# Kernel optimization log

Hardware: AMD Instinct MI355X
Metric: run time of the kernel (lower is better)

## Reference

```python
import jax, jax.numpy as jnp
import numpy as np

VAR0, VAR1 = 0.1, 0.2       # variances used by encode()
THRESH = 0.35               # overlap_thresh
NEGPOS = 7                  # negpos_ratio


def point_form(p):
    # (cx,cy,w,h) -> (xmin,ymin,xmax,ymax)
    return jnp.concatenate([p[:, :2] - p[:, 2:] / 2, p[:, :2] + p[:, 2:] / 2], axis=1)


def jaccard(a, b):
    # a:[G,4], b:[P,4] corner form -> IoU [G,P]
    lt = jnp.maximum(a[:, None, :2], b[None, :, :2])
    rb = jnp.minimum(a[:, None, 2:], b[None, :, 2:])
    wh = jnp.clip(rb - lt, 0.0, None)
    inter = wh[..., 0] * wh[..., 1]
    area_a = (a[:, 2] - a[:, 0]) * (a[:, 3] - a[:, 1])
    area_b = (b[:, 2] - b[:, 0]) * (b[:, 3] - b[:, 1])
    return inter / (area_a[:, None] + area_b[None, :] - inter)


def encode(matched, priors):
    g_cxcy = ((matched[:, :2] + matched[:, 2:]) / 2 - priors[:, :2]) / (VAR0 * priors[:, 2:])
    g_wh = jnp.log((matched[:, 2:] - matched[:, :2]) / priors[:, 2:]) / VAR1
    return jnp.concatenate([g_cxcy, g_wh], axis=1)


def encode_landm(matched, priors):
    m = matched.reshape(-1, 5, 2)                                  # [P,5,2]
    g = (m - priors[:, None, :2]) / (VAR0 * priors[:, None, 2:])
    return g.reshape(-1, 10)


def match_one(truths, labels, landms, priors, priors_pf):
    # truths:[G,4] labels:[G] landms:[G,10] priors:[P,4](cxcywh) priors_pf:[P,4](corner)
    G = truths.shape[0]
    P = priors.shape[0]
    ov = jaccard(truths, priors_pf)                                # [G,P]
    best_prior_ov = ov.max(axis=1)                                 # [G]
    best_prior_idx = ov.argmax(axis=1)                             # [G]
    valid_gt = best_prior_ov >= 0.2
    best_truth_ov = ov.max(axis=0)                                 # [P]
    best_truth_idx = ov.argmax(axis=0)                             # [P]
    # index_fill_(0, best_prior_idx[valid_gt], 2): 2 > any IoU, so max is equivalent
    forced_ov = jnp.zeros((P,), ov.dtype).at[best_prior_idx].max(jnp.where(valid_gt, 2.0, 0.0))
    best_truth_ov = jnp.maximum(best_truth_ov, forced_ov)
    forced_idx = jnp.full((P,), -1, jnp.int32).at[best_prior_idx].max(jnp.arange(G, dtype=jnp.int32))
    best_truth_idx = jnp.where(forced_idx >= 0, forced_idx, best_truth_idx.astype(jnp.int32))
    conf = labels[best_truth_idx].astype(jnp.int32)
    conf = jnp.where(best_truth_ov < THRESH, 0, conf)
    loc = encode(truths[best_truth_idx], priors)                   # [P,4]
    landm = encode_landm(landms[best_truth_idx], priors)           # [P,10]
    # if no valid gt, torch zeroes the targets for this sample
    any_valid = valid_gt.any()
    loc = jnp.where(any_valid, loc, 0.0)
    landm = jnp.where(any_valid, landm, 0.0)
    conf = jnp.where(any_valid, conf, 0)
    return loc, conf, landm


def smooth_l1(x):
    ax = jnp.abs(x)
    return jnp.where(ax < 1.0, 0.5 * ax * ax, ax - 0.5)


def setup_inputs() -> dict:
    key = jax.random.key(0)
    k1, k2, k3, k4, k5, k6, k7, k8, k9 = jax.random.split(key, 9)
    B, P, G, C = 64, 16800, 32, 2
    cls_data = jax.random.normal(k1, (B, P, C), jnp.float32)
    loc_data = jax.random.normal(k2, (B, P, 4), jnp.float32)
    landm_data = jax.random.normal(k3, (B, P, 10), jnp.float32)
    # priors in (cx,cy,w,h), w,h in [0.02,0.3]
    pc = jax.random.uniform(k4, (P, 2), jnp.float32)
    pwh = jax.random.uniform(k5, (P, 2), jnp.float32, 0.02, 0.3)
    priors = jnp.concatenate([pc, pwh], axis=1)
    # targets: [B,G,15] = 4 box (corner form, valid) + 10 landmarks + 1 label
    c = jax.random.uniform(k6, (B, G, 2), jnp.float32, 0.15, 0.85)
    s = jax.random.uniform(k7, (B, G, 2), jnp.float32, 0.02, 0.3)
    boxes = jnp.concatenate([c - s / 2, c + s / 2], axis=-1)
    lms = jax.random.uniform(k8, (B, G, 10), jnp.float32)
    labels = jnp.where(jax.random.uniform(k9, (B, G, 1)) < 0.3, -1.0, 1.0)
    targets = jnp.concatenate([boxes, lms, labels], axis=-1)
    return {"cls_data": cls_data, "loc_data": loc_data, "landm_data": landm_data,
            "priors": priors, "targets": targets}


def reference(cls_data, loc_data, landm_data, priors, targets):
    truths = targets[:, :, :4]
    landms = targets[:, :, 4:14]
    labels = targets[:, :, 14]
    priors_pf = point_form(priors)
    loc_t, conf_t, landm_t = jax.vmap(
        lambda t, l, lm: match_one(t, l, lm, priors, priors_pf))(truths, labels, landms)
    num, P = conf_t.shape

    # landmark loss (smooth L1 over conf_t > 0)
    pos1 = conf_t > 0
    N1 = jnp.maximum(pos1.sum().astype(jnp.float32), 1.0)
    loss_landm = jnp.sum(smooth_l1(landm_data - landm_t) * pos1[..., None].astype(landm_data.dtype))

    # localization loss (smooth L1 over conf_t != 0)
    pos = conf_t != 0
    conf_t = jnp.where(pos, 1, conf_t)                              # conf_t[pos] = 1
    loss_l = jnp.sum(smooth_l1(loc_data - loc_t) * pos[..., None].astype(loc_data.dtype))

    # hard negative mining on per-prior CE loss
    logz = jax.nn.logsumexp(cls_data, axis=-1)                      # [B,P]
    gold = jnp.take_along_axis(cls_data, conf_t[..., None], axis=-1)[..., 0]
    loss_c = jnp.where(pos, 0.0, logz - gold)
    loss_idx = jnp.argsort(-loss_c, axis=1)
    idx_rank = jnp.argsort(loss_idx, axis=1)
    num_pos = pos.sum(axis=1, keepdims=True)
    num_neg = jnp.clip(NEGPOS * num_pos, None, P - 1)
    neg = idx_rank < num_neg

    sel = (pos | neg).astype(cls_data.dtype)
    loss_conf = jnp.sum((logz - gold) * sel)

    N = jnp.maximum(num_pos.sum().astype(jnp.float32), 1.0)
    return loss_l / N, loss_conf / N, loss_landm / N1
```

## Files before the change

### kernel.cpp

```cpp
#include <hip/hip_runtime.h>
#include <hip/hip_bf16.h>
#include <math.h>


#define RCP(x) __builtin_amdgcn_rcpf(x)
typedef unsigned long long u64;

constexpr int GN = 32;
constexpr int PACKF = 576;

__device__ __forceinline__ float sl1(float x) {
    float a = fabsf(x);
    return a < 1.f ? 0.5f * a * a : a - 0.5f;
}

constexpr int GPB = 4;
constexpr int GNT = 1024;
__global__ __launch_bounds__(GNT)
void k_gt(const float4* __restrict__ priors, const float* __restrict__ targets,
          u64* __restrict__ keys, float* __restrict__ pack,
          int* __restrict__ done, int P, int G) {
    const int b = blockIdx.y, g0 = blockIdx.x * GPB, tid = threadIdx.x;
    const int lane = tid & 63, w = tid >> 6;
    if (blockIdx.x == 0 && blockIdx.y == 0 && tid == 0) *done = 0;
    __shared__ float4 s_box[GPB];
    __shared__ float  s_at[GPB];
    __shared__ u64 s_wk[GNT / 64][GPB];
    if (tid < GPB) {
        const float* t = targets + ((size_t)b * G + g0 + tid) * 15;
        float4 v = make_float4(t[0], t[1], t[2], t[3]);
        float at = (v.z - v.x) * (v.w - v.y);
        s_box[tid] = v;
        s_at[tid] = at;
        float* pk = pack + (size_t)b * PACKF;
        ((float4*)pk)[g0 + tid] = v;
        pk[128 + g0 + tid] = 0.35f * at;
        pk[160 + g0 + tid] = at;
        pk[192 + g0 + tid] = t[14];
    }
    {
        int q = tid - GPB;
        if (q >= 0 && q < GPB * 10) {
            int gg = g0 + q / 10, j = q % 10;
            pack[(size_t)b * PACKF + 224 + gg * 10 + j] =
                targets[((size_t)b * G + gg) * 15 + 4 + j];
        }
    }
    __syncthreads();
    float4 tb0 = s_box[0], tb1 = s_box[1], tb2 = s_box[2], tb3 = s_box[3];
    float at0 = s_at[0], at1 = s_at[1], at2 = s_at[2], at3 = s_at[3];

    float bv[GPB]; int bp[GPB];
    #pragma unroll
    for (int j = 0; j < GPB; ++j) { bv[j] = -1.f; bp[j] = 0; }

    for (int p = tid; p < P; p += GNT) {
        float4 pr = priors[p];
        float hx = pr.z * 0.5f, hy = pr.w * 0.5f;
        float px0 = pr.x - hx, py0 = pr.y - hy;
        float px1 = pr.x + hx, py1 = pr.y + hy;
        float ap = (px1 - px0) * (py1 - py0);
        #pragma unroll
        for (int j = 0; j < GPB; ++j) {
            float4 tb = j == 0 ? tb0 : (j == 1 ? tb1 : (j == 2 ? tb2 : tb3));
            float at = j == 0 ? at0 : (j == 1 ? at1 : (j == 2 ? at2 : at3));
            float lx = fmaxf(tb.x, px0), ly = fmaxf(tb.y, py0);
            float rx = fminf(tb.z, px1), ry = fminf(tb.w, py1);
            float iw = fmaxf(rx - lx, 0.f), ih = fmaxf(ry - ly, 0.f);
            float inter = iw * ih;
            float iou = inter * RCP(at + ap - inter);
            if (iou > bv[j]) { bv[j] = iou; bp[j] = p; }
        }
    }
    #pragma unroll
    for (int j = 0; j < GPB; ++j) {
        u64 key = ((u64)__float_as_uint(bv[j]) << 32) | ~(unsigned)bp[j];
        #pragma unroll
        for (int o = 32; o > 0; o >>= 1) {
            u64 t = __shfl_down(key, o, 64);
            if (t > key) key = t;
        }
        if (lane == 0) s_wk[w][j] = key;
    }
    __syncthreads();
    if (tid < GPB) {
        u64 m = 0ull;
        #pragma unroll
        for (int q = 0; q < GNT / 64; ++q) { u64 t = s_wk[q][tid]; if (t > m) m = t; }
        keys[b * G + g0 + tid] = m;
    }
}

__global__ __launch_bounds__(256)
void k_match(const float2* __restrict__ cls, const float4* __restrict__ loc,
             const float* __restrict__ lmd, const float4* __restrict__ priors,
             const float* __restrict__ pack, const u64* __restrict__ keys,
             float* __restrict__ bc, float* __restrict__ part, int P, int NB) {
    const int b = blockIdx.y, bx = blockIdx.x, tid = threadIdx.x;
    const int lane = tid & 63, w = tid >> 6;
    const float* __restrict__ pk = pack + (size_t)b * PACKF;
    const float4* __restrict__ gbox = (const float4*)pk;
    const float* __restrict__ gc35 = pk + 128;
    const float* __restrict__ garea = pk + 160;
    const float* __restrict__ glab = pk + 192;
    const float* __restrict__ glm  = pk + 224;

    __shared__ int s_fg[256];
    __shared__ int s_fv[256];
    __shared__ unsigned s_vm;
    __shared__ float s_red[4][8];

    s_fg[tid] = -1; s_fv[tid] = 0;
    __syncthreads();
    if (tid < GN) {
        u64 key = keys[b * GN + tid];
        unsigned bp = ~(unsigned)key;
        bool val = __uint_as_float((unsigned)(key >> 32)) >= 0.2f;
        u64 bal = __ballot(val);
        if (tid == 0) s_vm = (unsigned)bal;
        int local = (int)bp - bx * 256;
        if (local >= 0 && local < 256) {
            atomicMax(&s_fg[local], tid);
            if (val) atomicOr(&s_fv[local], 1);
        }
    }
    __syncthreads();
    const bool av = s_vm != 0u;

    int p = bx * 256 + tid;
    const bool act = p < P;
    float2 c = act ? cls[(size_t)b * P + p] : make_float2(0.f, 0.f);
    float4 pr = act ? priors[p] : make_float4(0.f, 0.f, 0.f, 0.f);
    float hx = pr.z * 0.5f, hy = pr.w * 0.5f;
    float px0 = pr.x - hx, py0 = pr.y - hy;
    float px1 = pr.x + hx, py1 = pr.y + hy;
    float ap = (px1 - px0) * (py1 - py0);
    float ap35 = 0.35f * ap;

    float qmax = -INFINITY;
    #pragma unroll
    for (int g = 0; g < GN; ++g) {
        float4 tb = gbox[g];
        float lx = fmaxf(tb.x, px0), ly = fmaxf(tb.y, py0);
        float rx = fminf(tb.z, px1), ry = fminf(tb.w, py1);
        float iw = fmaxf(rx - lx, 0.f), ih = fmaxf(ry - ly, 0.f);
        qmax = fmaxf(qmax, fmaf(1.35f, iw * ih, -gc35[g]));
    }
    bool thr = act && (qmax >= ap35);
    int fidx = s_fg[tid];
    bool fv = s_fv[tid] != 0;
    bool pos = act && av && (fv || thr);

    float lse = 0.f, d = 0.f;
    if (act) {
        d = c.y - c.x;
        float m0 = fmaxf(d, 0.f);
        lse = m0 + __logf(__expf(-m0) + __expf(d - m0));
        bc[(size_t)b * P + p] = pos ? 0.f : lse;
    }

    float a_ll = 0.f, a_lm = 0.f, a_lcp = 0.f;
    bool posl = false;
    if (pos) {
        a_lcp = lse - d;
        int bti2 = fidx;
        if (fidx < 0) {
            float btv = -1.f;
            #pragma unroll 1
            for (int g = 0; g < GN; ++g) {
                float4 tb = gbox[g];
                float lx = fmaxf(tb.x, px0), ly = fmaxf(tb.y, py0);
                float rx = fminf(tb.z, px1), ry = fminf(tb.w, py1);
                float iw = fmaxf(rx - lx, 0.f), ih = fmaxf(ry - ly, 0.f);
                float inter = iw * ih;
                float iou = inter * RCP(garea[g] + ap - inter);
                if (iou > btv) { btv = iou; bti2 = g; }
            }
        }
        float4 tb = gbox[bti2];
        float rw = RCP(pr.z), rh = RCP(pr.w);
        float e0 = ((tb.x + tb.z) * 0.5f - pr.x) * rw * 10.f;
        float e1 = ((tb.y + tb.w) * 0.5f - pr.y) * rh * 10.f;
        float e2 = __logf((tb.z - tb.x) * rw) * 5.f;
        float e3 = __logf((tb.w - tb.y) * rh) * 5.f;
        float4 ld = loc[(size_t)b * P + p];
        a_ll = sl1(ld.x - e0) + sl1(ld.y - e1) + sl1(ld.z - e2) + sl1(ld.w - e3);
        if (glab[bti2] > 0.f) {
            posl = true;
            const float* lp = lmd + ((size_t)b * P + p) * 10;
            #pragma unroll
            for (int q = 0; q < 5; ++q) {
                float gx = (glm[bti2 * 10 + 2 * q]     - pr.x) * rw * 10.f;
                float gy = (glm[bti2 * 10 + 2 * q + 1] - pr.y) * rh * 10.f;
                a_lm += sl1(lp[2 * q] - gx) + sl1(lp[2 * q + 1] - gy);
            }
        }
    }

    u64 bpos = __ballot(pos);
    int npw  = __popcll(bpos);
    int np1w = __popcll(__ballot(posl));
    if (bpos) {
        #pragma unroll
        for (int o = 32; o > 0; o >>= 1) {
            a_ll  += __shfl_down(a_ll,  o, 64);
            a_lm  += __shfl_down(a_lm,  o, 64);
            a_lcp += __shfl_down(a_lcp, o, 64);
        }
    }
    if (lane == 0) {
        s_red[w][0] = a_ll; s_red[w][1] = a_lm; s_red[w][2] = a_lcp;
        s_red[w][3] = (float)npw; s_red[w][4] = (float)np1w;
    }
    __syncthreads();
    if (tid == 0) {
        float* pp = part + ((size_t)b * NB + bx) * 8;
        #pragma unroll
        for (int j = 0; j < 5; ++j)
            pp[j] = s_red[0][j] + s_red[1][j] + s_red[2][j] + s_red[3][j];
    }
}

constexpr int KNT = 1024;
constexpr int KNI = 17;
__global__ __launch_bounds__(KNT)
void k_select(const float* __restrict__ bc, const float* __restrict__ part,
              float* __restrict__ part2, float* __restrict__ out,
              int* __restrict__ done, int P, int NB, int B) {
    const int b = blockIdx.x, tid = threadIdx.x;
    const int lane = tid & 63, w = tid >> 6;
    __shared__ float s_r[5];
    __shared__ u64   s_cw[16];
    __shared__ u64   s_ct;
    __shared__ float s_rf[16][2];
    __shared__ float s_ts2[2];
    __shared__ int   s_last;

    unsigned ul[KNI];
    #pragma unroll
    for (int i = 0; i < KNI; ++i) {
        int idx = i * KNT + tid;
        ul[i] = idx < P ? __float_as_uint(bc[(size_t)b * P + idx]) : 0u;
    }
    if (w < 5) {
        float s = 0.f;
        for (int bx = lane; bx < NB; bx += 64) s += part[((size_t)b * NB + bx) * 8 + w];
        #pragma unroll
        for (int o = 32; o > 0; o >>= 1) s += __shfl_down(s, o, 64);
        if (lane == 0) s_r[w] = s;
    }
    __syncthreads();
    const float t_ll = s_r[0], t_lm = s_r[1], t_lcp = s_r[2];
    const float t_np = s_r[3], t_np1 = s_r[4];
    int k = (int)(t_np + 0.5f) * 7;
    if (k > P - 1) k = P - 1;

    float topk = 0.f;
    if (k > 0) {
        unsigned lo = 0u, hi = 0x7f800000u;
        while (lo < hi) {
            unsigned span = hi - lo;
            unsigned m1 = lo + ((span + 3) >> 2);
            unsigned m2 = lo + ((span + 1) >> 1);
            unsigned m3 = hi - (span >> 2);
            int c1 = 0, c2 = 0, c3 = 0;
            #pragma unroll
            for (int i = 0; i < KNI; ++i) {
                unsigned u = ul[i];
                c1 += u >= m1 ? 1 : 0;
                c2 += u >= m2 ? 1 : 0;
                c3 += u >= m3 ? 1 : 0;
            }
            u64 pk = (u64)c1 | ((u64)c2 << 20) | ((u64)c3 << 40);
            #pragma unroll
            for (int o = 32; o > 0; o >>= 1) pk += __shfl_down(pk, o, 64);
            if (lane == 0) s_cw[w] = pk;
            __syncthreads();
            if (w == 0) {
                u64 t = (lane < 16) ? s_cw[lane] : 0ull;
                #pragma unroll
                for (int o = 8; o > 0; o >>= 1) t += __shfl_down(t, o, 64);
                if (lane == 0) s_ct = t;
            }
            __syncthreads();
            u64 t = s_ct;
            int C1 = (int)(t & 0xFFFFFu);
            int C2 = (int)((t >> 20) & 0xFFFFFu);
            int C3 = (int)((t >> 40) & 0xFFFFFu);
            if      (C3 >= k) lo = m3;
            else if (C2 >= k) { lo = m2; hi = m3 - 1; }
            else if (C1 >= k) { lo = m1; hi = m2 - 1; }
            else hi = m1 - 1;
        }
        float fT = __uint_as_float(lo);
        float s = 0.f, cf = 0.f;
        #pragma unroll
        for (int i = 0; i < KNI; ++i)
            if (ul[i] > lo) { s += __uint_as_float(ul[i]); cf += 1.f; }
        #pragma unroll
        for (int o = 32; o > 0; o >>= 1) {
            s  += __shfl_down(s, o, 64);
            cf += __shfl_down(cf, o, 64);
        }
        if (lane == 0) { s_rf[w][0] = s; s_rf[w][1] = cf; }
        __syncthreads();
        if (w == 0) {
            float a = (lane < 16) ? s_rf[lane][0] : 0.f;
            float bb = (lane < 16) ? s_rf[lane][1] : 0.f;
            #pragma unroll
            for (int o = 8; o > 0; o >>= 1) {
                a  += __shfl_down(a, o, 64);
                bb += __shfl_down(bb, o, 64);
            }
            if (lane == 0) { s_ts2[0] = a; s_ts2[1] = bb; }
        }
        __syncthreads();
        topk = s_ts2[0] + ((float)k - s_ts2[1]) * fT;
    }
    if (tid == 0) {
        float* pp = part2 + b * 8;
        pp[0] = t_ll; pp[1] = t_lm; pp[2] = t_lcp;
        pp[3] = topk; pp[4] = t_np; pp[5] = t_np1;
        __threadfence();
        int old = atomicAdd(done, 1);
        s_last = (old == B - 1) ? 1 : 0;
    }
    __syncthreads();
    if (s_last && w == 0) {
        __threadfence();
        volatile float* vp = part2;
        float ll = 0.f, lm = 0.f, lc = 0.f, tk = 0.f, np = 0.f, np1 = 0.f;
        for (int bb = lane; bb < B; bb += 64) {
            ll  += vp[bb * 8 + 0];
            lm  += vp[bb * 8 + 1];
            lc  += vp[bb * 8 + 2];
            tk  += vp[bb * 8 + 3];
            np  += vp[bb * 8 + 4];
            np1 += vp[bb * 8 + 5];
        }
        #pragma unroll
        for (int o = 32; o > 0; o >>= 1) {
            ll  += __shfl_down(ll,  o, 64);
            lm  += __shfl_down(lm,  o, 64);
            lc  += __shfl_down(lc,  o, 64);
            tk  += __shfl_down(tk,  o, 64);
            np  += __shfl_down(np,  o, 64);
            np1 += __shfl_down(np1, o, 64);
        }
        if (lane == 0) {
            float N = fmaxf(np, 1.f), N1 = fmaxf(np1, 1.f);
            out[0] = ll / N;
            out[1] = (lc + tk) / N;
            out[2] = lm / N1;
        }
    }
}

extern "C" void kernel_launch(void* const* d_in, const int* in_sizes, int n_in,
                              void* d_out, int out_size, void* d_ws, size_t ws_size,
                              hipStream_t stream) {
    const float2* cls    = (const float2*)d_in[0];
    const float4* loc    = (const float4*)d_in[1];
    const float* lmd     = (const float*)d_in[2];
    const float4* priors = (const float4*)d_in[3];
    const float* targets = (const float*)d_in[4];
    int P = in_sizes[3] / 4;
    int B = (in_sizes[1] / 4) / P;
    int G = in_sizes[4] / (15 * B);
    int NB = (P + 255) / 256;

    size_t off = 0;
    u64* keys    = (u64*)d_ws;                     off += (size_t)B * G * 8;
    float* pack  = (float*)((char*)d_ws + off);    off += (size_t)B * PACKF * 4;
    float* part  = (float*)((char*)d_ws + off);    off += (size_t)B * NB * 8 * 4;
    float* part2 = (float*)((char*)d_ws + off);    off += (size_t)B * 8 * 4;
    int* done    = (int*)((char*)d_ws + off);      off += 256;
    off = (off + 255) & ~(size_t)255;
    float* bc    = (float*)((char*)d_ws + off);

    dim3 ggt((G + GPB - 1) / GPB, B);
    k_gt<<<ggt, GNT, 0, stream>>>(priors, targets, keys, pack, done, P, G);
    dim3 gm(NB, B);
    k_match<<<gm, 256, 0, stream>>>(cls, loc, lmd, priors, pack, keys, bc, part, P, NB);
    k_select<<<B, KNT, 0, stream>>>(bc, part, part2, (float*)d_out, done, P, NB, B);
}
```

Measured before the change: 94.61 us.

## Transpose threshold IoU test to lane-per-GT with ballot-based prior masks

The per-prior loop over all 32 GT boxes in k_match is replaced by a layout where each lane holds one GT box and each half-wave tests one prior per iteration. Wave ballots combine the results into a 64-bit mask of priors that pass the 0.35 overlap threshold. This removes the serial 32-iteration loop of uniform GT loads per thread, but adds 32 ballot iterations per wave with redundant prior loads and recomputation of prior corners. Prior geometry is now loaded only for positive priors. The loop is also moved ahead of the __syncthreads, so it can overlap with the shared-memory setup.

```diff
diff --git a/kernel.cpp b/kernel.cpp
--- a/kernel.cpp
+++ b/kernel.cpp
@@ -32,11 +32,11 @@
         float at = (v.z - v.x) * (v.w - v.y);
         s_box[tid] = v;
         s_at[tid] = at;
-        float* pk = pack + (size_t)b * PACKF;
-        ((float4*)pk)[g0 + tid] = v;
-        pk[128 + g0 + tid] = 0.35f * at;
-        pk[160 + g0 + tid] = at;
-        pk[192 + g0 + tid] = t[14];
+        float* pkw = pack + (size_t)b * PACKF;
+        ((float4*)pkw)[g0 + tid] = v;
+        pkw[128 + g0 + tid] = 0.35f * at;
+        pkw[160 + g0 + tid] = at;
+        pkw[192 + g0 + tid] = t[14];
     }
     {
         int q = tid - GPB;
@@ -100,7 +100,6 @@
     const int lane = tid & 63, w = tid >> 6;
     const float* __restrict__ pk = pack + (size_t)b * PACKF;
     const float4* __restrict__ gbox = (const float4*)pk;
-    const float* __restrict__ gc35 = pk + 128;
     const float* __restrict__ garea = pk + 160;
     const float* __restrict__ glab = pk + 192;
     const float* __restrict__ glm  = pk + 224;
@@ -124,29 +123,37 @@
             if (val) atomicOr(&s_fv[local], 1);
         }
     }
-    __syncthreads();
-    const bool av = s_vm != 0u;
 
     int p = bx * 256 + tid;
     const bool act = p < P;
     float2 c = act ? cls[(size_t)b * P + p] : make_float2(0.f, 0.f);
-    float4 pr = act ? priors[p] : make_float4(0.f, 0.f, 0.f, 0.f);
-    float hx = pr.z * 0.5f, hy = pr.w * 0.5f;
-    float px0 = pr.x - hx, py0 = pr.y - hy;
-    float px1 = pr.x + hx, py1 = pr.y + hy;
-    float ap = (px1 - px0) * (py1 - py0);
-    float ap35 = 0.35f * ap;
-
-    float qmax = -INFINITY;
-    #pragma unroll
-    for (int g = 0; g < GN; ++g) {
-        float4 tb = gbox[g];
-        float lx = fmaxf(tb.x, px0), ly = fmaxf(tb.y, py0);
-        float rx = fminf(tb.z, px1), ry = fminf(tb.w, py1);
+
+    const int gl = lane & 31, half = lane >> 5;
+    float4 gtb = gbox[gl];
+    float gc = pk[128 + gl];
+    const int pbase = bx * 256 + w * 64;
+    u64 thrm = 0ull;
+    #pragma unroll 8
+    for (int i = 0; i < 32; ++i) {
+        int p2 = pbase + 2 * i + half;
+        bool a2 = p2 < P;
+        float4 pr2 = a2 ? priors[p2] : make_float4(0.f, 0.f, 0.f, 0.f);
+        float hx = pr2.z * 0.5f, hy = pr2.w * 0.5f;
+        float qx0 = pr2.x - hx, qy0 = pr2.y - hy;
+        float qx1 = pr2.x + hx, qy1 = pr2.y + hy;
+        float ap35 = 0.35f * ((qx1 - qx0) * (qy1 - qy0));
+        float lx = fmaxf(gtb.x, qx0), ly = fmaxf(gtb.y, qy0);
+        float rx = fminf(gtb.z, qx1), ry = fminf(gtb.w, qy1);
         float iw = fmaxf(rx - lx, 0.f), ih = fmaxf(ry - ly, 0.f);
-        qmax = fmaxf(qmax, fmaf(1.35f, iw * ih, -gc35[g]));
-    }
-    bool thr = act && (qmax >= ap35);
+        bool pass = a2 && (fmaf(1.35f, iw * ih, -gc) >= ap35);
+        u64 bal = __ballot(pass);
+        thrm |= (u64)((bal & 0xFFFFFFFFull) != 0ull) << (2 * i);
+        thrm |= (u64)((bal >> 32) != 0ull) << (2 * i + 1);
+    }
+    __syncthreads();
+    const bool av = s_vm != 0u;
+
+    bool thr = act && ((thrm >> lane) & 1ull);
     int fidx = s_fg[tid];
     bool fv = s_fv[tid] != 0;
     bool pos = act && av && (fv || thr);
@@ -163,6 +170,11 @@
     bool posl = false;
     if (pos) {
         a_lcp = lse - d;
+        float4 pr = priors[p];
+        float hx = pr.z * 0.5f, hy = pr.w * 0.5f;
+        float px0 = pr.x - hx, py0 = pr.y - hy;
+        float px1 = pr.x + hx, py1 = pr.y + hy;
+        float ap = (px1 - px0) * (py1 - py0);
         int bti2 = fidx;
         if (fidx < 0) {
             float btv = -1.f;
@@ -271,10 +283,10 @@
                 c2 += u >= m2 ? 1 : 0;
                 c3 += u >= m3 ? 1 : 0;
             }
-            u64 pk = (u64)c1 | ((u64)c2 << 20) | ((u64)c3 << 40);
+            u64 pkk = (u64)c1 | ((u64)c2 << 20) | ((u64)c3 << 40);
             #pragma unroll
-            for (int o = 32; o > 0; o >>= 1) pk += __shfl_down(pk, o, 64);
-            if (lane == 0) s_cw[w] = pk;
+            for (int o = 32; o > 0; o >>= 1) pkk += __shfl_down(pkk, o, 64);
+            if (lane == 0) s_cw[w] = pkk;
             __syncthreads();
             if (w == 0) {
                 u64 t = (lane < 16) ? s_cw[lane] : 0ull;
```

Result: slower. 111.5 us (+17.8%).
